# Optimization experiments

Measured on AMD Instinct MI355X. Metric: run time of the kernel, lower is better.

The kernel has to match this reference:

```python
import jax, jax.numpy as jnp
import numpy as np
import math

B, C, H, T, S = 2, 1024, 16, 2048, 2048
DH = C // H  # 64


def setup_inputs() -> dict:
    key = jax.random.key(0)
    ks = jax.random.split(key, 10)
    target = jax.random.normal(ks[0], (B, C, T), dtype=jnp.float32)
    source = jax.random.normal(ks[1], (B, C, S), dtype=jnp.float32)
    target_mask = (jax.random.uniform(ks[2], (B, 1, T)) < 0.9).astype(jnp.float32)
    source_mask = (jax.random.uniform(ks[3], (B, 1, S)) < 0.9).astype(jnp.float32)
    scale = 1.0 / math.sqrt(C)
    Wq = jax.random.normal(ks[4], (C, C), dtype=jnp.float32) * scale
    bq = jnp.zeros((C,), dtype=jnp.float32)
    Wk = jax.random.normal(ks[5], (C, C), dtype=jnp.float32) * scale
    bk = jnp.zeros((C,), dtype=jnp.float32)
    Wv = jax.random.normal(ks[6], (C, C), dtype=jnp.float32) * scale
    bv = jnp.zeros((C,), dtype=jnp.float32)
    return {"target": target, "source": source, "target_mask": target_mask,
            "source_mask": source_mask, "Wq": Wq, "bq": bq, "Wk": Wk, "bk": bk,
            "Wv": Wv, "bv": bv}


def _proj(W, b, x):
    # 1x1 Conv1d == pointwise channel mixing: [B,C,L] -> [B,C,L]
    return jnp.einsum('oc,bcl->bol', W, x) + b[None, :, None]


def reference(target, source, target_mask, source_mask, Wq, bq, Wk, bk, Wv, bv):
    q = _proj(Wq, bq, target).reshape(B, H, DH, T)
    k = _proj(Wk, bk, source).reshape(B, H, DH, S)
    v = _proj(Wv, bv, source).reshape(B, H, DH, S)
    # dot: [B,H,T,S], scaled by sqrt(d_head) (key.size(2) in torch)
    dot = jnp.einsum('bhdt,bhds->bhts', q, k) / math.sqrt(DH)
    # available mask [B,1,T,S], broadcast over heads
    avail = jnp.einsum('bjt,bjs->bjts', target_mask, source_mask)
    dot = avail * dot - (1.0 - avail) * 1.0e6
    # NOTE: original torch code overwrites the masked amap with a plain
    # softmax of the (masked) dot; we reproduce that exactly.
    amap = jax.nn.softmax(dot, axis=-1)
    out = jnp.einsum('bhts,bhds->bhdt', amap, v)  # [B,H,DH,T]
    return out.reshape(B, C, T)
```

## Files before the change

### kernel.cpp

```cpp
#include <hip/hip_runtime.h>

#define BB 2
#define CC 1024
#define HH 16
#define TT 2048
#define SS 2048
#define LL 2048
#define C2MASK 1442695.0f
#define NT_TILES (SS / 64)

typedef unsigned short u16;
typedef unsigned int u32;
typedef __attribute__((ext_vector_type(8))) short short8;
typedef __attribute__((ext_vector_type(4))) float f32x4;
typedef __attribute__((ext_vector_type(4))) unsigned short us4;
typedef __attribute__((ext_vector_type(2))) unsigned int u32x2;
typedef __attribute__((ext_vector_type(4))) unsigned int u32x4;

__device__ __forceinline__ u16 f2bf(float f) {
    union { float f; unsigned int i; } x; x.f = f;
    unsigned int r = x.i + 0x7FFFu + ((x.i >> 16) & 1u);
    return (u16)(r >> 16);
}
__device__ __forceinline__ float exp2_hw(float x) {
    float r;
    asm("v_exp_f32 %0, %1" : "=v"(r) : "v"(x));
    return r;
}
__device__ __forceinline__ float max3f(float a, float b, float c) {
    float r;
    asm("v_max3_f32 %0, %1, %2, %3" : "=v"(r) : "v"(a), "v"(b), "v"(c));
    return r;
}
__device__ __forceinline__ u32 cvtpk_bf16(float lo, float hi) {
    u32 r;
    asm("v_cvt_pk_bf16_f32 %0, %1, %2" : "=v"(r) : "v"(lo), "v"(hi));
    return r;
}
__device__ __forceinline__ void gload_lds16(const u16* g, u16* l) {
    __builtin_amdgcn_global_load_lds(
        (const __attribute__((address_space(1))) unsigned int*)g,
        (__attribute__((address_space(3))) unsigned int*)l, 16, 0, 0);
}

__global__ __launch_bounds__(256) void prep(
    const float* __restrict__ target, const float* __restrict__ source,
    const float* __restrict__ smaskp,
    const float* __restrict__ Wq, const float* __restrict__ Wk, const float* __restrict__ Wv,
    u16* __restrict__ Wb, u16* __restrict__ Tt, u16* __restrict__ St,
    float* __restrict__ sbias, float* __restrict__ zrow)
{
    __shared__ float xs[64][65];
    const int tid = threadIdx.x;
    const int bid = blockIdx.x;

    if (bid < 2048) {
        const int img  = bid >> 9;
        const int tile = bid & 511;
        const int ct = tile >> 5, lt = tile & 31;
        const int c0 = ct * 64, l0 = lt * 64;
        const float* src = ((img < 2) ? target : source) + (size_t)(img & 1) * CC * LL;
        u16* dst = ((img < 2) ? Tt : St) + (size_t)(img & 1) * LL * CC;

        const int i = tid >> 2, seg = (tid & 3) * 16;
        const float* g = src + (size_t)(c0 + i) * LL + l0 + seg;
        f32x4 a0 = *(const f32x4*)g;
        f32x4 a1 = *(const f32x4*)(g + 4);
        f32x4 a2 = *(const f32x4*)(g + 8);
        f32x4 a3 = *(const f32x4*)(g + 12);
#pragma unroll
        for (int j = 0; j < 4; j++) {
            xs[i][seg + j]      = a0[j];
            xs[i][seg + 4 + j]  = a1[j];
            xs[i][seg + 8 + j]  = a2[j];
            xs[i][seg + 12 + j] = a3[j];
        }
        __syncthreads();

        const int l = tid >> 2, cseg = (tid & 3) * 16;
        float f[16];
#pragma unroll
        for (int j = 0; j < 16; j++) f[j] = xs[cseg + j][l];
        u32x4 o0, o1;
#pragma unroll
        for (int k = 0; k < 4; k++) {
            o0[k] = cvtpk_bf16(f[2 * k], f[2 * k + 1]);
            o1[k] = cvtpk_bf16(f[8 + 2 * k], f[9 + 2 * k]);
        }
        u16* d = dst + (size_t)(l0 + l) * CC + c0 + cseg;
        *(u32x4*)d = o0;
        *(u32x4*)(d + 8) = o1;
    } else {
        const int wblk = bid - 2048;
        const size_t idx = (size_t)wblk * 2048 + tid * 8;
        const int m = (int)(idx >> 20);
        const size_t rem = idx & 1048575;
        const float* srcp = ((m == 0) ? Wq : (m == 1) ? Wk : Wv) + rem;
        f32x4 a = *(const f32x4*)srcp;
        f32x4 c = *(const f32x4*)(srcp + 4);
        u32x4 o;
        o[0] = cvtpk_bf16(a[0], a[1]); o[1] = cvtpk_bf16(a[2], a[3]);
        o[2] = cvtpk_bf16(c[0], c[1]); o[3] = cvtpk_bf16(c[2], c[3]);
        *(u32x4*)(Wb + ((size_t)m << 20) + rem) = o;

        if (wblk < 2) {
            const int b = wblk;
            const float* sm = smaskp + (size_t)b * SS;
            float* sb = sbias + (size_t)b * SS;
            for (int s = tid; s < SS; s += 256) {
                sb[s] = (sm[s] > 0.5f) ? 0.0f : -C2MASK;
                if (b == 0) zrow[s] = 0.0f;
            }
        }
    }
}

__global__ __launch_bounds__(256) void qkv_gemm(
    const u16* __restrict__ Wb, const u16* __restrict__ Tt, const u16* __restrict__ St,
    const float* __restrict__ bq, const float* __restrict__ bk, const float* __restrict__ bv,
    const float* __restrict__ tmaskp,
    u16* __restrict__ Qb, u16* __restrict__ Kb, u16* __restrict__ Vb)
{
    __shared__ __align__(16) u16 As[3][4096];
    __shared__ __align__(16) u16 Bs[3][4096];

    const int p = blockIdx.z >> 1;
    const int b = blockIdx.z & 1;
    const int m0 = blockIdx.y * 128;
    const int n0 = blockIdx.x * 128;

    const u16* A  = Wb + ((size_t)p << 20) + (size_t)m0 * CC;
    const u16* Bx = ((p == 0) ? Tt : St) + (size_t)b * LL * CC + (size_t)n0 * CC;
    const float* bias = (p == 0) ? bq : (p == 1) ? bk : bv;

    const int tid  = threadIdx.x;
    const int lane = tid & 63;
    const int wid  = tid >> 6;
    const int ln   = lane & 15;
    const int q    = lane >> 4;
    const int wm   = (wid >> 1) * 64;
    const int wn   = (wid & 1) * 64;

    int row1, c1, row2, c2;
    { const int s = tid;       const int pp = s >> 3, j = s & 7, i = j ^ (pp & 7);
      row1 = 2 * pp + (i >> 2); c1 = i & 3; }
    { const int s = tid + 256; const int pp = s >> 3, j = s & 7, i = j ^ (pp & 7);
      row2 = 2 * pp + (i >> 2); c2 = i & 3; }
    const u16* ag1 = A  + (size_t)row1 * CC + c1 * 8;
    const u16* ag2 = A  + (size_t)row2 * CC + c2 * 8;
    const u16* bg1 = Bx + (size_t)row1 * CC + c1 * 8;
    const u16* bg2 = Bx + (size_t)row2 * CC + c2 * 8;
    const int lb = wid * 512;

#define QSTAGE(buf, k0) do {                                  \
        gload_lds16(ag1 + (k0), &As[buf][lb]);                \
        gload_lds16(ag2 + (k0), &As[buf][2048 + lb]);         \
        gload_lds16(bg1 + (k0), &Bs[buf][lb]);                \
        gload_lds16(bg2 + (k0), &Bs[buf][2048 + lb]);         \
    } while (0)

    f32x4 acc[4][4];
#pragma unroll
    for (int i = 0; i < 4; i++)
#pragma unroll
        for (int j = 0; j < 4; j++) acc[i][j] = (f32x4){0.f, 0.f, 0.f, 0.f};

    const int loff = (ln >> 1) * 64 + (((((ln & 1) << 2) | q)) ^ (ln >> 1)) * 8;

    QSTAGE(0, 0);
    QSTAGE(1, 32);

    int cur = 0;
    for (int k0 = 0; k0 < CC; k0 += 32) {
        if (k0 < CC - 32) { asm volatile("s_waitcnt vmcnt(4)" ::: "memory"); }
        else              { asm volatile("s_waitcnt vmcnt(0)" ::: "memory"); }
        __builtin_amdgcn_s_barrier();
        __builtin_amdgcn_sched_barrier(0);

        int nxt = cur + 2; if (nxt >= 3) nxt -= 3;
        if (k0 + 64 < CC) QSTAGE(nxt, k0 + 64);

        short8 aF[4], bF[4];
#pragma unroll
        for (int mt = 0; mt < 4; mt++)
            aF[mt] = *(const short8*)(&As[cur][wm * 32 + mt * 512 + loff]);
#pragma unroll
        for (int nt = 0; nt < 4; nt++)
            bF[nt] = *(const short8*)(&Bs[cur][wn * 32 + nt * 512 + loff]);
#pragma unroll
        for (int mt = 0; mt < 4; mt++)
#pragma unroll
            for (int nt = 0; nt < 4; nt++)
                acc[mt][nt] = __builtin_amdgcn_mfma_f32_16x16x32_bf16(aF[mt], bF[nt], acc[mt][nt], 0, 0, 0);
        cur = (cur == 2) ? 0 : cur + 1;
    }
#undef QSTAGE

    const float oscale = (p == 0) ? 0.18033688011112042f : 1.0f;
#pragma unroll
    for (int mt = 0; mt < 4; mt++) {
        const int o_base = m0 + wm + mt * 16 + q * 4;
        float bsf[4];
#pragma unroll
        for (int r = 0; r < 4; r++) bsf[r] = bias[o_base + r];
#pragma unroll
        for (int nt = 0; nt < 4; nt++) {
            const int l = n0 + wn + nt * 16 + ln;
            if (p == 2) {
#pragma unroll
                for (int r = 0; r < 4; r++)
                    Vb[((size_t)b * CC + o_base + r) * SS + l] = f2bf(acc[mt][nt][r] + bsf[r]);
            } else {
                const int h = o_base >> 6;
                const int d = o_base & 63;
                u16* dst = (p == 0) ? Qb : Kb;
                float sc2 = oscale;
                if (p == 0) sc2 = oscale * tmaskp[(size_t)b * TT + l];
                us4 pk;
#pragma unroll
                for (int r = 0; r < 4; r++) pk[r] = (u16)f2bf((acc[mt][nt][r] + bsf[r]) * sc2);
                *(us4*)(dst + ((size_t)(b * HH + h) * TT + l) * 64 + d) = pk;
            }
        }
    }
}

__global__ __launch_bounds__(512, 4) void attn_k(
    const u16* __restrict__ Qb, const u16* __restrict__ Kb, const u16* __restrict__ Vb,
    const float* __restrict__ tmask, const float* __restrict__ sbias,
    const float* __restrict__ zrow, float* __restrict__ out)
{
    __shared__ __align__(16) u16 Ks[2][64 * 64];
    __shared__ __align__(16) u16 Vs[2][64 * 64];
    __shared__ __align__(16) u16 Ps[8][16 * 64];

    const int tid  = threadIdx.x;
    const int wid  = tid >> 6;
    const int lane = tid & 63;
    const int ln   = lane & 15;
    const int q    = lane >> 4;

    const int idx   = blockIdx.x;
    const int xcd   = idx & 7;
    const int rest  = idx >> 3;
    const int ttile = rest & 15;
    const int bh    = (rest >> 4) * 8 + xcd;
    const int b     = bh >> 4;
    const int h     = bh & 15;
    const int t0    = ttile * 128 + wid * 16;

    const u16* Qp = Qb + (size_t)bh * TT * 64;
    const u16* Kp = Kb + (size_t)bh * SS * 64;
    const u16* Vp = Vb + ((size_t)b * CC + h * 64) * SS;

    const float tm = tmask[(size_t)b * TT + t0 + ln];
    const float* bp = (tm > 0.5f) ? (sbias + (size_t)b * SS) : zrow;

    const int r0  = tid >> 3;
    const int c0  = tid & 7;
    const int cs0 = c0 ^ (r0 & 7);
    const u16* kg = Kp + (size_t)r0 * 64 + cs0 * 8;
    const u16* vg = Vp + (size_t)r0 * SS + cs0 * 8;
    const int lws = wid * 512;

#define STAGE(buf, sn) do {                                 \
        gload_lds16(kg + (size_t)(sn) * 64, &Ks[buf][lws]); \
        gload_lds16(vg + (sn), &Vs[buf][lws]);              \
    } while (0)

    short8 qB0 = *(const short8*)(Qp + (size_t)(t0 + ln) * 64 + q * 8);
    short8 qB1 = *(const short8*)(Qp + (size_t)(t0 + ln) * 64 + 32 + q * 8);

    float mR = -3.0e38f, lR = 0.f;
    f32x4 oA[4];
#pragma unroll
    for (int dt = 0; dt < 4; dt++) oA[dt] = (f32x4){0.f, 0.f, 0.f, 0.f};

    const int sx0 = ((q ^ (ln & 7)) << 3);
    const int sx1 = (((q + 4) ^ (ln & 7)) << 3);

    u16* pw = Ps[wid];

    STAGE(0, 0);

    int cur = 0;
#pragma unroll 2
    for (int it = 0; it < NT_TILES; ++it) {
        const int s0 = it * 64;
        __syncthreads();
        if (it + 1 < NT_TILES) STAGE(cur ^ 1, s0 + 64);

        const u16* KsB = Ks[cur];
        const u16* VsB = Vs[cur];

        f32x4 sc[4];
        __builtin_amdgcn_s_setprio(1);
#pragma unroll
        for (int nt = 0; nt < 4; nt++) {
            const u16* kr = KsB + (nt * 16 + ln) * 64;
            short8 k0 = *(const short8*)(kr + sx0);
            short8 k1 = *(const short8*)(kr + sx1);
            f32x4 bias = *(const f32x4*)(bp + s0 + nt * 16 + q * 4);
            sc[nt] = __builtin_amdgcn_mfma_f32_16x16x32_bf16(k0, qB0, bias, 0, 0, 0);
            sc[nt] = __builtin_amdgcn_mfma_f32_16x16x32_bf16(k1, qB1, sc[nt], 0, 0, 0);
        }
        __builtin_amdgcn_s_setprio(0);

        float m4[4];
#pragma unroll
        for (int nt = 0; nt < 4; nt++)
            m4[nt] = fmaxf(max3f(sc[nt][0], sc[nt][1], sc[nt][2]), sc[nt][3]);
        float m_ = fmaxf(max3f(m4[0], m4[1], m4[2]), m4[3]);
        m_ = fmaxf(m_, __shfl_xor(m_, 16, 64));
        m_ = fmaxf(m_, __shfl_xor(m_, 32, 64));

        if (!__all(m_ - mR <= 8.0f)) {
            const float mN = fmaxf(mR, m_);
            const float al = exp2_hw(mR - mN);
            lR *= al;
#pragma unroll
            for (int dt = 0; dt < 4; dt++) oA[dt] *= al;
            mR = mN;
        }

        float s4[4];
#pragma unroll
        for (int nt = 0; nt < 4; nt++) {
#pragma unroll
            for (int r = 0; r < 4; r++) sc[nt][r] = exp2_hw(sc[nt][r] - mR);
            s4[nt] = (sc[nt][0] + sc[nt][1]) + (sc[nt][2] + sc[nt][3]);
        }
        float s_ = (s4[0] + s4[1]) + (s4[2] + s4[3]);
        s_ += __shfl_xor(s_, 16, 64);
        s_ += __shfl_xor(s_, 32, 64);
        lR += s_;

#pragma unroll
        for (int nt = 0; nt < 4; nt++) {
            u32x2 w;
            w[0] = cvtpk_bf16(sc[nt][0], sc[nt][1]);
            w[1] = cvtpk_bf16(sc[nt][2], sc[nt][3]);
            const int chunk = (nt << 1) | (q >> 1);
            *(u32x2*)(pw + ln * 64 + ((chunk ^ (ln & 7)) << 3) + ((q & 1) << 2)) = w;
        }
        short8 pB0 = *(const short8*)(pw + ln * 64 + sx0);
        short8 pB1 = *(const short8*)(pw + ln * 64 + sx1);
        __builtin_amdgcn_s_setprio(1);
#pragma unroll
        for (int dt = 0; dt < 4; dt++) {
            const u16* vr = VsB + (dt * 16 + ln) * 64;
            short8 v0 = *(const short8*)(vr + sx0);
            short8 v1 = *(const short8*)(vr + sx1);
            oA[dt] = __builtin_amdgcn_mfma_f32_16x16x32_bf16(v0, pB0, oA[dt], 0, 0, 0);
            oA[dt] = __builtin_amdgcn_mfma_f32_16x16x32_bf16(v1, pB1, oA[dt], 0, 0, 0);
        }
        __builtin_amdgcn_s_setprio(0);
        cur ^= 1;
    }
#undef STAGE

    const float inv = 1.0f / lR;
#pragma unroll
    for (int dt = 0; dt < 4; dt++)
#pragma unroll
        for (int r = 0; r < 4; r++)
            out[((size_t)b * CC + h * 64 + dt * 16 + q * 4 + r) * TT + t0 + ln] =
                oA[dt][r] * inv;
}

extern "C" void kernel_launch(void* const* d_in, const int* in_sizes, int n_in,
                              void* d_out, int out_size, void* d_ws, size_t ws_size,
                              hipStream_t stream)
{
    const float* target = (const float*)d_in[0];
    const float* source = (const float*)d_in[1];
    const float* tmask  = (const float*)d_in[2];
    const float* smask  = (const float*)d_in[3];
    const float* Wq = (const float*)d_in[4];
    const float* bq = (const float*)d_in[5];
    const float* Wk = (const float*)d_in[6];
    const float* bk = (const float*)d_in[7];
    const float* Wv = (const float*)d_in[8];
    const float* bv = (const float*)d_in[9];

    u16* ws = (u16*)d_ws;
    const size_t N1 = (size_t)BB * CC * TT;
    u16* Qb = ws;
    u16* Kb = ws + N1;
    u16* Vb = ws + 2 * N1;
    float* sbias = (float*)(ws + 3 * N1);
    float* zrow  = sbias + 2 * SS;
    u16* Wb = (u16*)(zrow + SS);
    u16* Tt = Wb + 3u * 1048576u;
    u16* St = Tt + (size_t)BB * LL * CC;

    prep<<<dim3(3584, 1, 1), dim3(256, 1, 1), 0, stream>>>(
        target, source, smask, Wq, Wk, Wv, Wb, Tt, St, sbias, zrow);
    qkv_gemm<<<dim3(TT/128, CC/128, 6), dim3(256, 1, 1), 0, stream>>>(
        Wb, Tt, St, bq, bk, bv, tmask, Qb, Kb, Vb);
    attn_k<<<dim3(BB*HH*(TT/128), 1, 1), dim3(512, 1, 1), 0, stream>>>(
        Qb, Kb, Vb, tmask, sbias, zrow, (float*)d_out);
}
```

Measured before the change: 208.4 us.

## Enlarge QKV GEMM tiles to 256x256 with 512 threads and XCD-aware block mapping

The QKV projection GEMM moves from 128x128 tiles with 256 threads and a triple-buffered K=32 pipeline to 256x256 tiles with 512 threads, double-buffered K=64 stages, and a flattened grid of 192 blocks. The three projections and both batches are folded into one M/N index space, and block IDs are remapped so neighbouring tiles spread across XCDs. The larger tiles raise arithmetic intensity and cut redundant global loads. In exchange the kernel uses more LDS and registers per block, leaving fewer blocks per CU, and 192 blocks may leave the 256 CUs partly idle.

```diff
diff --git a/kernel.cpp b/kernel.cpp
--- a/kernel.cpp
+++ b/kernel.cpp
@@ -115,22 +115,25 @@
     }
 }
 
-__global__ __launch_bounds__(256) void qkv_gemm(
+__global__ __launch_bounds__(512, 2) void qkv_gemm(
     const u16* __restrict__ Wb, const u16* __restrict__ Tt, const u16* __restrict__ St,
     const float* __restrict__ bq, const float* __restrict__ bk, const float* __restrict__ bv,
     const float* __restrict__ tmaskp,
     u16* __restrict__ Qb, u16* __restrict__ Kb, u16* __restrict__ Vb)
 {
-    __shared__ __align__(16) u16 As[3][4096];
-    __shared__ __align__(16) u16 Bs[3][4096];
-
-    const int p = blockIdx.z >> 1;
-    const int b = blockIdx.z & 1;
-    const int m0 = blockIdx.y * 128;
-    const int n0 = blockIdx.x * 128;
-
-    const u16* A  = Wb + ((size_t)p << 20) + (size_t)m0 * CC;
-    const u16* Bx = ((p == 0) ? Tt : St) + (size_t)b * LL * CC + (size_t)n0 * CC;
+    __shared__ __align__(16) u16 As[2][16384];
+    __shared__ __align__(16) u16 Bs[2][16384];
+
+    const int orig = blockIdx.x;
+    const int wg   = (orig & 7) * 24 + (orig >> 3);
+    const int mT   = wg >> 4;
+    const int nT   = wg & 15;
+    const int m0 = mT * 256;
+    const int n0 = nT * 256;
+    const int p  = m0 >> 10;
+
+    const u16* A  = Wb + (size_t)m0 * CC;
+    const u16* Bx = ((p == 0) ? Tt : St) + (size_t)n0 * CC;
     const float* bias = (p == 0) ? bq : (p == 1) ? bk : bv;
 
     const int tid  = threadIdx.x;
@@ -138,88 +141,98 @@
     const int wid  = tid >> 6;
     const int ln   = lane & 15;
     const int q    = lane >> 4;
-    const int wm   = (wid >> 1) * 64;
-    const int wn   = (wid & 1) * 64;
-
-    int row1, c1, row2, c2;
-    { const int s = tid;       const int pp = s >> 3, j = s & 7, i = j ^ (pp & 7);
-      row1 = 2 * pp + (i >> 2); c1 = i & 3; }
-    { const int s = tid + 256; const int pp = s >> 3, j = s & 7, i = j ^ (pp & 7);
-      row2 = 2 * pp + (i >> 2); c2 = i & 3; }
-    const u16* ag1 = A  + (size_t)row1 * CC + c1 * 8;
-    const u16* ag2 = A  + (size_t)row2 * CC + c2 * 8;
-    const u16* bg1 = Bx + (size_t)row1 * CC + c1 * 8;
-    const u16* bg2 = Bx + (size_t)row2 * CC + c2 * 8;
-    const int lb = wid * 512;
-
-#define QSTAGE(buf, k0) do {                                  \
-        gload_lds16(ag1 + (k0), &As[buf][lb]);                \
-        gload_lds16(ag2 + (k0), &As[buf][2048 + lb]);         \
-        gload_lds16(bg1 + (k0), &Bs[buf][lb]);                \
-        gload_lds16(bg2 + (k0), &Bs[buf][2048 + lb]);         \
+    const int wm   = (wid >> 2) * 128;
+    const int wn   = (wid & 3) * 64;
+
+    const u16* ag[4]; const u16* bg[4];
+#pragma unroll
+    for (int e = 0; e < 4; e++) {
+        const int s = tid + e * 512;
+        const int row = s >> 3;
+        const int c = (s & 7) ^ (row & 7);
+        ag[e] = A  + (size_t)row * CC + c * 8;
+        bg[e] = Bx + (size_t)row * CC + c * 8;
+    }
+    const int lw = wid * 512;
+
+#define QSTAGE(buf, k0) do {                                   \
+        gload_lds16(ag[0] + (k0), &As[buf][lw]);               \
+        gload_lds16(ag[1] + (k0), &As[buf][4096 + lw]);        \
+        gload_lds16(ag[2] + (k0), &As[buf][8192 + lw]);        \
+        gload_lds16(ag[3] + (k0), &As[buf][12288 + lw]);       \
+        gload_lds16(bg[0] + (k0), &Bs[buf][lw]);               \
+        gload_lds16(bg[1] + (k0), &Bs[buf][4096 + lw]);        \
+        gload_lds16(bg[2] + (k0), &Bs[buf][8192 + lw]);        \
+        gload_lds16(bg[3] + (k0), &Bs[buf][12288 + lw]);       \
     } while (0)
 
-    f32x4 acc[4][4];
-#pragma unroll
-    for (int i = 0; i < 4; i++)
+    f32x4 acc[8][4];
+#pragma unroll
+    for (int i = 0; i < 8; i++)
 #pragma unroll
         for (int j = 0; j < 4; j++) acc[i][j] = (f32x4){0.f, 0.f, 0.f, 0.f};
 
-    const int loff = (ln >> 1) * 64 + (((((ln & 1) << 2) | q)) ^ (ln >> 1)) * 8;
+    const int sx0 = ((q ^ (ln & 7)) << 3);
+    const int sx1 = (((q + 4) ^ (ln & 7)) << 3);
 
     QSTAGE(0, 0);
-    QSTAGE(1, 32);
 
     int cur = 0;
-    for (int k0 = 0; k0 < CC; k0 += 32) {
-        if (k0 < CC - 32) { asm volatile("s_waitcnt vmcnt(4)" ::: "memory"); }
-        else              { asm volatile("s_waitcnt vmcnt(0)" ::: "memory"); }
-        __builtin_amdgcn_s_barrier();
-        __builtin_amdgcn_sched_barrier(0);
-
-        int nxt = cur + 2; if (nxt >= 3) nxt -= 3;
-        if (k0 + 64 < CC) QSTAGE(nxt, k0 + 64);
-
-        short8 aF[4], bF[4];
-#pragma unroll
-        for (int mt = 0; mt < 4; mt++)
-            aF[mt] = *(const short8*)(&As[cur][wm * 32 + mt * 512 + loff]);
-#pragma unroll
-        for (int nt = 0; nt < 4; nt++)
-            bF[nt] = *(const short8*)(&Bs[cur][wn * 32 + nt * 512 + loff]);
-#pragma unroll
-        for (int mt = 0; mt < 4; mt++)
-#pragma unroll
-            for (int nt = 0; nt < 4; nt++)
-                acc[mt][nt] = __builtin_amdgcn_mfma_f32_16x16x32_bf16(aF[mt], bF[nt], acc[mt][nt], 0, 0, 0);
-        cur = (cur == 2) ? 0 : cur + 1;
+    for (int ks = 0; ks < 16; ++ks) {
+        __syncthreads();
+        if (ks + 1 < 16) QSTAGE(cur ^ 1, (ks + 1) * 64);
+
+        const u16* AsB = As[cur];
+        const u16* BsB = Bs[cur];
+
+        short8 bF[4][2];
+#pragma unroll
+        for (int nt = 0; nt < 4; nt++) {
+            const u16* br = BsB + (wn + nt * 16 + ln) * 64;
+            bF[nt][0] = *(const short8*)(br + sx0);
+            bF[nt][1] = *(const short8*)(br + sx1);
+        }
+#pragma unroll
+        for (int mt = 0; mt < 8; mt++) {
+            const u16* ar = AsB + (wm + mt * 16 + ln) * 64;
+            short8 a0 = *(const short8*)(ar + sx0);
+            short8 a1 = *(const short8*)(ar + sx1);
+#pragma unroll
+            for (int nt = 0; nt < 4; nt++) {
+                acc[mt][nt] = __builtin_amdgcn_mfma_f32_16x16x32_bf16(a0, bF[nt][0], acc[mt][nt], 0, 0, 0);
+                acc[mt][nt] = __builtin_amdgcn_mfma_f32_16x16x32_bf16(a1, bF[nt][1], acc[mt][nt], 0, 0, 0);
+            }
+        }
+        cur ^= 1;
     }
 #undef QSTAGE
 
-    const float oscale = (p == 0) ? 0.18033688011112042f : 1.0f;
-#pragma unroll
-    for (int mt = 0; mt < 4; mt++) {
-        const int o_base = m0 + wm + mt * 16 + q * 4;
+    const float oscale = 0.18033688011112042f;
+#pragma unroll
+    for (int mt = 0; mt < 8; mt++) {
+        const int o_base = (m0 & 1023) + wm + mt * 16 + q * 4;
         float bsf[4];
 #pragma unroll
         for (int r = 0; r < 4; r++) bsf[r] = bias[o_base + r];
 #pragma unroll
         for (int nt = 0; nt < 4; nt++) {
-            const int l = n0 + wn + nt * 16 + ln;
+            const int l  = n0 + wn + nt * 16 + ln;
+            const int b  = l >> 11;
+            const int tk = l & 2047;
             if (p == 2) {
 #pragma unroll
                 for (int r = 0; r < 4; r++)
-                    Vb[((size_t)b * CC + o_base + r) * SS + l] = f2bf(acc[mt][nt][r] + bsf[r]);
+                    Vb[((size_t)b * CC + o_base + r) * SS + tk] = f2bf(acc[mt][nt][r] + bsf[r]);
             } else {
                 const int h = o_base >> 6;
                 const int d = o_base & 63;
                 u16* dst = (p == 0) ? Qb : Kb;
-                float sc2 = oscale;
-                if (p == 0) sc2 = oscale * tmaskp[(size_t)b * TT + l];
+                float sc2 = 1.0f;
+                if (p == 0) sc2 = oscale * tmaskp[(size_t)b * TT + tk];
                 us4 pk;
 #pragma unroll
                 for (int r = 0; r < 4; r++) pk[r] = (u16)f2bf((acc[mt][nt][r] + bsf[r]) * sc2);
-                *(us4*)(dst + ((size_t)(b * HH + h) * TT + l) * 64 + d) = pk;
+                *(us4*)(dst + ((size_t)(b * HH + h) * TT + tk) * 64 + d) = pk;
             }
         }
     }
@@ -396,7 +409,7 @@
 
     prep<<<dim3(3584, 1, 1), dim3(256, 1, 1), 0, stream>>>(
         target, source, smask, Wq, Wk, Wv, Wb, Tt, St, sbias, zrow);
-    qkv_gemm<<<dim3(TT/128, CC/128, 6), dim3(256, 1, 1), 0, stream>>>(
+    qkv_gemm<<<dim3(192, 1, 1), dim3(512, 1, 1), 0, stream>>>(
         Wb, Tt, St, bq, bk, bv, tmask, Qb, Kb, Vb);
     attn_k<<<dim3(BB*HH*(TT/128), 1, 1), dim3(512, 1, 1), 0, stream>>>(
         Qb, Kb, Vb, tmask, sbias, zrow, (float*)d_out);
```

New measurement: 202.8 us. 1.03x faster.
